# Performance work log

Hardware: AMD Instinct MI355X
Metric: run time of the kernel (lower is better)

Reference implementation:

```python
import jax, jax.numpy as jnp
import numpy as np

COMMITMENT_COST = 0.25


def setup_inputs() -> dict:
    key = jax.random.key(0)
    k1, k2 = jax.random.split(key)
    z = jax.random.normal(k1, (16, 64, 64, 64), dtype=jnp.float32)  # [B, C=embed_dim, H, W]
    embedding = jax.random.normal(k2, (1024, 64), dtype=jnp.float32)  # [K, D]
    return {"z": z, "embedding": embedding}


def reference(z, embedding):
    B, C, H, W = z.shape
    K, D = embedding.shape
    # NCHW -> NHWC, flatten to [N, D]
    z_perm = jnp.transpose(z, (0, 2, 3, 1))
    z_flat = z_perm.reshape(-1, D)
    N = z_flat.shape[0]
    # squared L2 distances: ||z||^2 + ||e||^2 - 2 z e^T  -> [N, K]
    distances = (
        jnp.sum(z_flat ** 2, axis=1, keepdims=True)
        + jnp.sum(embedding ** 2, axis=1)
        - 2.0 * jnp.matmul(z_flat, embedding.T)
    )
    encoding_indices = jnp.argmin(distances, axis=1)  # [N]
    # gather instead of one-hot matmul (same math, efficient)
    quantized = embedding[encoding_indices].reshape(z_perm.shape)
    # commitment loss (eval-mode forward; EMA buffer updates are train-only side effects)
    e_latent_loss = jnp.mean((jax.lax.stop_gradient(quantized) - z_perm) ** 2)
    loss = COMMITMENT_COST * e_latent_loss
    # straight-through estimator
    quantized_st = z_perm + jax.lax.stop_gradient(quantized - z_perm)
    quantized_out = jnp.transpose(quantized_st, (0, 3, 1, 2))
    # perplexity from code usage histogram (== mean of one-hot encodings)
    avg_probs = jnp.zeros((K,), dtype=jnp.float32).at[encoding_indices].add(1.0) / N
    perplexity = jnp.exp(-jnp.sum(avg_probs * jnp.log(avg_probs + 1e-10)))
    return quantized_out, loss, encoding_indices.reshape(B, H, W), perplexity
```

## Files before the change

### kernel.cpp

```cpp
#include <hip/hip_runtime.h>
#include <math.h>


#define QOUT_SZ  4194304
#define LOSS_OFF QOUT_SZ
#define IDX_OFF  (QOUT_SZ + 1)
#define PERP_OFF (QOUT_SZ + 1 + 65536)

typedef _Float16 f16x8 __attribute__((ext_vector_type(8)));
typedef _Float16 f16x4 __attribute__((ext_vector_type(4)));
typedef float    f32x4 __attribute__((ext_vector_type(4)));

#define WS_EHI   0
#define WS_ELO   131072
#define WS_ESQ   262144
#define WS_HIST  266240
#define WS_LOSS  270336

__device__ __forceinline__ void gll16(const void* g, void* l) {
    __builtin_amdgcn_global_load_lds(
        (const __attribute__((address_space(1))) void*)g,
        (__attribute__((address_space(3))) void*)l, 16, 0, 0);
}

__global__ void vq_pre(const float* __restrict__ emb,
                       _Float16* __restrict__ ehi, _Float16* __restrict__ elo,
                       float* __restrict__ esq, float* __restrict__ hist) {
    const int t = threadIdx.x;
    const int g = blockIdx.x * 256 + t;
    float4 v = ((const float4*)emb)[g];
    float xs[4] = {v.x, v.y, v.z, v.w};
    f16x4 hi, lo;
    float ss = 0.f;
#pragma unroll
    for (int j = 0; j < 4; ++j) {
        _Float16 h = (_Float16)xs[j];
        hi[j] = h;
        lo[j] = (_Float16)((xs[j] - (float)h) * 4096.0f);
        ss = fmaf(xs[j], xs[j], ss);
    }
    ((f16x4*)ehi)[g] = hi;
    ((f16x4*)elo)[g] = lo;
    ss += __shfl_xor(ss, 1, 64);
    ss += __shfl_xor(ss, 2, 64);
    ss += __shfl_xor(ss, 4, 64);
    ss += __shfl_xor(ss, 8, 64);
    if ((t & 15) == 0) esq[g >> 4] = -0.5f * ss;
    if (blockIdx.x < 4) hist[blockIdx.x * 256 + t] = 0.f;
}

__launch_bounds__(256, 4)
__global__ void vq_main(const float* __restrict__ z,
                        const float* __restrict__ emb,
                        const _Float16* __restrict__ gehi,
                        const _Float16* __restrict__ gelo,
                        const float* __restrict__ gesq,
                        float* __restrict__ hist,
                        float* __restrict__ lossp,
                        float* __restrict__ out) {
    __shared__ __align__(16) char es[32768];
    __shared__ float esql[1024];
    __shared__ float candv[128];
    __shared__ int   candi[128];
    __shared__ int   idxs[64];
    __shared__ float redw[4];

    const int tid  = threadIdx.x;
    const int blk  = blockIdx.x;
    const int b    = blk >> 6;
    const int h    = blk & 63;
    const int lane = tid & 63;
    const int wv   = tid >> 6;
    const int pg   = wv & 1;
    const int ksel = wv >> 1;
    const int col  = lane & 15;
    const int g    = lane >> 4;

#pragma unroll
    for (int i = 0; i < 4; ++i) esql[tid + 256 * i] = gesq[tid + 256 * i];

    const float* zb = z + (size_t)b * 262144 + (size_t)h * 64;
    const float* zrow = zb + pg * 32 + col;
    f16x8 Ah[2][2], Al[2][2];
#pragma unroll
    for (int pt = 0; pt < 2; ++pt) {
#pragma unroll
        for (int m = 0; m < 2; ++m) {
#pragma unroll
            for (int j = 0; j < 8; ++j) {
                int c = m * 32 + g * 8 + j;
                float x = zrow[pt * 16 + (size_t)c * 4096];
                _Float16 hh = (_Float16)x;
                Ah[pt][m][j] = hh;
                Al[pt][m][j] = (_Float16)((x - (float)hh) * 4096.0f);
            }
        }
    }

    const char* gh = (const char*)gehi;
    const char* gl = (const char*)gelo;
    const int u0 = tid, u1 = tid + 256;
    const int c0 = u0 >> 3, c1 = u1 >> 3;
    const size_t so0 = (size_t)c0 * 128 + (size_t)(((u0 & 7) ^ (c0 & 7)) * 16);
    const size_t so1 = (size_t)c1 * 128 + (size_t)(((u1 & 7) ^ (c1 & 7)) * 16);
    char* const dA = es + wv * 1024;

#define STAGE(n, bb) do { \
        const size_t gb_ = (size_t)(n) * 8192; \
        char* d_ = dA + (bb) * 16384; \
        gll16(gh + gb_ + so0, d_);            \
        gll16(gh + gb_ + so1, d_ + 4096);     \
        gll16(gl + gb_ + so0, d_ + 8192);     \
        gll16(gl + gb_ + so1, d_ + 12288);    \
    } while (0)

    int rb[2][2];
#pragma unroll
    for (int ct = 0; ct < 2; ++ct) {
        int cl = ksel * 32 + ct * 16 + col;
#pragma unroll
        for (int m = 0; m < 2; ++m)
            rb[ct][m] = cl * 128 + ((((m * 4 + g) * 16)) ^ ((col & 7) << 4));
    }

    float best[2][4];
    int   besti[2][4];
#pragma unroll
    for (int pt = 0; pt < 2; ++pt)
#pragma unroll
        for (int r = 0; r < 4; ++r) { best[pt][r] = -3.4e38f; besti[pt][r] = 0; }

    STAGE(0, 0);

    for (int sc = 0; sc < 16; ++sc) {
        const int cur = sc & 1;
        asm volatile("s_waitcnt vmcnt(0)" ::: "memory");
        __builtin_amdgcn_s_barrier();
        asm volatile("" ::: "memory");
        if (sc < 15) STAGE(sc + 1, cur ^ 1);

        const char* bp = es + cur * 16384;
        const int kb = sc * 64 + ksel * 32;
#pragma unroll
        for (int ct = 0; ct < 2; ++ct) {
            const float e2  = esql[kb + ct * 16 + col];
            const int  kidx = kb + ct * 16 + col;
            f16x8 Bh0 = *(const f16x8*)(bp + rb[ct][0]);
            f16x8 Bh1 = *(const f16x8*)(bp + rb[ct][1]);
            f16x8 Bl0 = *(const f16x8*)(bp + 8192 + rb[ct][0]);
            f16x8 Bl1 = *(const f16x8*)(bp + 8192 + rb[ct][1]);
#pragma unroll
            for (int pt = 0; pt < 2; ++pt) {
                f32x4 ah = {e2, e2, e2, e2};
                f32x4 ax = {0.f, 0.f, 0.f, 0.f};
                ah = __builtin_amdgcn_mfma_f32_16x16x32_f16(Ah[pt][0], Bh0, ah, 0, 0, 0);
                ah = __builtin_amdgcn_mfma_f32_16x16x32_f16(Ah[pt][1], Bh1, ah, 0, 0, 0);
                ax = __builtin_amdgcn_mfma_f32_16x16x32_f16(Ah[pt][0], Bl0, ax, 0, 0, 0);
                ax = __builtin_amdgcn_mfma_f32_16x16x32_f16(Ah[pt][1], Bl1, ax, 0, 0, 0);
                ax = __builtin_amdgcn_mfma_f32_16x16x32_f16(Al[pt][0], Bh0, ax, 0, 0, 0);
                ax = __builtin_amdgcn_mfma_f32_16x16x32_f16(Al[pt][1], Bh1, ax, 0, 0, 0);
#pragma unroll
                for (int r = 0; r < 4; ++r) {
                    float mval = fmaf(0x1p-12f, ax[r], ah[r]);
                    if (mval > best[pt][r]) { best[pt][r] = mval; besti[pt][r] = kidx; }
                }
            }
        }
    }
#undef STAGE

#pragma unroll
    for (int mask = 1; mask <= 8; mask <<= 1) {
#pragma unroll
        for (int pt = 0; pt < 2; ++pt)
#pragma unroll
            for (int r = 0; r < 4; ++r) {
                float ov = __shfl_xor(best[pt][r], mask, 64);
                int   oi = __shfl_xor(besti[pt][r], mask, 64);
                if (ov > best[pt][r] ||
                    (ov == best[pt][r] && oi < besti[pt][r])) {
                    best[pt][r] = ov; besti[pt][r] = oi;
                }
            }
    }
    if (col == 0) {
#pragma unroll
        for (int pt = 0; pt < 2; ++pt)
#pragma unroll
            for (int r = 0; r < 4; ++r) {
                int p = pg * 32 + pt * 16 + g * 4 + r;
                candv[p * 2 + ksel] = best[pt][r];
                candi[p * 2 + ksel] = besti[pt][r];
            }
    }
    __syncthreads();

    if (tid < 64) {
        float v0 = candv[tid * 2],     v1 = candv[tid * 2 + 1];
        int   i0 = candi[tid * 2],     i1 = candi[tid * 2 + 1];
        int bi = (v1 > v0 || (v1 == v0 && i1 < i0)) ? i1 : i0;
        idxs[tid] = bi;
        atomicAdd(&hist[bi], 1.0f);
        out[(size_t)IDX_OFF + blk * 64 + tid] = (float)bi;
    }
    __syncthreads();

    const int w  = tid & 63;
    const int cq = tid >> 6;
    const int idx = idxs[w];
    const float* ev = emb + (size_t)idx * 64 + cq * 16;
    const float* zr = zb + w;
    float* outq = out + (size_t)b * 262144 + (size_t)h * 64 + w;
    float lsum = 0.f;
#pragma unroll
    for (int i = 0; i < 4; ++i) {
        float4 qv = *(const float4*)(ev + i * 4);
        float q4[4] = {qv.x, qv.y, qv.z, qv.w};
#pragma unroll
        for (int jj = 0; jj < 4; ++jj) {
            int c = cq * 16 + i * 4 + jj;
            float zv = zr[(size_t)c * 4096];
            outq[(size_t)c * 4096] = q4[jj];
            float d = q4[jj] - zv;
            lsum = fmaf(d, d, lsum);
        }
    }
#pragma unroll
    for (int off = 32; off > 0; off >>= 1)
        lsum += __shfl_xor(lsum, off, 64);
    if (lane == 0) redw[wv] = lsum;
    __syncthreads();
    if (tid == 0)
        lossp[blk] = redw[0] + redw[1] + redw[2] + redw[3];
}

__global__ void vq_fin(const float* __restrict__ hist,
                       const float* __restrict__ lossp,
                       float* __restrict__ out) {
    __shared__ float sh[1024];
    __shared__ float sl[1024];
    int t = threadIdx.x;
    float hc = hist[t];
    float p  = hc * (1.0f / 65536.0f);
    sh[t] = p * logf(p + 1e-10f);
    sl[t] = lossp[t];
    __syncthreads();
    for (int s = 512; s > 0; s >>= 1) {
        if (t < s) { sh[t] += sh[t + s]; sl[t] += sl[t + s]; }
        __syncthreads();
    }
    if (t == 0) {
        out[LOSS_OFF] = 0.25f * sl[0] / (float)QOUT_SZ;
        out[PERP_OFF] = expf(-sh[0]);
    }
}

extern "C" void kernel_launch(void* const* d_in, const int* in_sizes, int n_in,
                              void* d_out, int out_size, void* d_ws, size_t ws_size,
                              hipStream_t stream) {
    const float* z   = (const float*)d_in[0];
    const float* emb = (const float*)d_in[1];
    float* out = (float*)d_out;
    char*  ws  = (char*)d_ws;

    _Float16* ehi   = (_Float16*)(ws + WS_EHI);
    _Float16* elo   = (_Float16*)(ws + WS_ELO);
    float*    esq   = (float*)(ws + WS_ESQ);
    float*    hist  = (float*)(ws + WS_HIST);
    float*    lossp = (float*)(ws + WS_LOSS);

    vq_pre<<<64, 256, 0, stream>>>(emb, ehi, elo, esq, hist);
    vq_main<<<1024, 256, 0, stream>>>(z, emb, ehi, elo, esq, hist, lossp, out);
    vq_fin<<<1, 1024, 0, stream>>>(hist, lossp, out);
}
```

Measured before the change: 67.55 us.

## Enlarge VQ block to 256 points with triple-buffered codebook staging

```diff
diff --git a/kernel.cpp b/kernel.cpp
--- a/kernel.cpp
+++ b/kernel.cpp
@@ -49,7 +49,7 @@
     if (blockIdx.x < 4) hist[blockIdx.x * 256 + t] = 0.f;
 }
 
-__launch_bounds__(256, 4)
+__launch_bounds__(512, 2)
 __global__ void vq_main(const float* __restrict__ z,
                         const float* __restrict__ emb,
                         const _Float16* __restrict__ gehi,
@@ -58,38 +58,39 @@
                         float* __restrict__ hist,
                         float* __restrict__ lossp,
                         float* __restrict__ out) {
-    __shared__ __align__(16) char es[32768];
+    __shared__ __align__(16) char es[49152];
     __shared__ float esql[1024];
-    __shared__ float candv[128];
-    __shared__ int   candi[128];
-    __shared__ int   idxs[64];
-    __shared__ float redw[4];
+
+    float* candv = (float*)es;
+    int*   candi = (int*)(es + 2048);
+    int*   idxs  = (int*)(es + 4096);
+    float* redw  = (float*)(es + 5120);
 
     const int tid  = threadIdx.x;
     const int blk  = blockIdx.x;
-    const int b    = blk >> 6;
-    const int h    = blk & 63;
+    const int b    = blk >> 4;
+    const int h0   = (blk & 15) << 2;
     const int lane = tid & 63;
     const int wv   = tid >> 6;
-    const int pg   = wv & 1;
-    const int ksel = wv >> 1;
+    const int q    = wv >> 1;
+    const int ksel = wv & 1;
     const int col  = lane & 15;
     const int g    = lane >> 4;
 
-#pragma unroll
-    for (int i = 0; i < 4; ++i) esql[tid + 256 * i] = gesq[tid + 256 * i];
-
-    const float* zb = z + (size_t)b * 262144 + (size_t)h * 64;
-    const float* zrow = zb + pg * 32 + col;
-    f16x8 Ah[2][2], Al[2][2];
-#pragma unroll
-    for (int pt = 0; pt < 2; ++pt) {
+    esql[tid]       = gesq[tid];
+    esql[tid + 512] = gesq[tid + 512];
+
+    const float* zb = z + (size_t)b * 262144 + (size_t)h0 * 64;
+    const float* zrw = zb + q * 64 + col;
+    f16x8 Ah[4][2], Al[4][2];
+#pragma unroll
+    for (int pt = 0; pt < 4; ++pt) {
 #pragma unroll
         for (int m = 0; m < 2; ++m) {
 #pragma unroll
             for (int j = 0; j < 8; ++j) {
                 int c = m * 32 + g * 8 + j;
-                float x = zrow[pt * 16 + (size_t)c * 4096];
+                float x = zrw[pt * 16 + (size_t)c * 4096];
                 _Float16 hh = (_Float16)x;
                 Ah[pt][m][j] = hh;
                 Al[pt][m][j] = (_Float16)((x - (float)hh) * 4096.0f);
@@ -99,19 +100,14 @@
 
     const char* gh = (const char*)gehi;
     const char* gl = (const char*)gelo;
-    const int u0 = tid, u1 = tid + 256;
-    const int c0 = u0 >> 3, c1 = u1 >> 3;
-    const size_t so0 = (size_t)c0 * 128 + (size_t)(((u0 & 7) ^ (c0 & 7)) * 16);
-    const size_t so1 = (size_t)c1 * 128 + (size_t)(((u1 & 7) ^ (c1 & 7)) * 16);
-    char* const dA = es + wv * 1024;
-
-#define STAGE(n, bb) do { \
+    const int   cc = tid >> 3;
+    const size_t so = (size_t)cc * 128 + (size_t)(((tid & 7) ^ (cc & 7)) << 4);
+    const int dofs = wv * 1024;
+
+#define STAGE(n, bo) do { \
         const size_t gb_ = (size_t)(n) * 8192; \
-        char* d_ = dA + (bb) * 16384; \
-        gll16(gh + gb_ + so0, d_);            \
-        gll16(gh + gb_ + so1, d_ + 4096);     \
-        gll16(gl + gb_ + so0, d_ + 8192);     \
-        gll16(gl + gb_ + so1, d_ + 12288);    \
+        gll16(gh + gb_ + so, es + (bo) + dofs);          \
+        gll16(gl + gb_ + so, es + (bo) + 8192 + dofs);   \
     } while (0)
 
     int rb[2][2];
@@ -120,37 +116,43 @@
         int cl = ksel * 32 + ct * 16 + col;
 #pragma unroll
         for (int m = 0; m < 2; ++m)
-            rb[ct][m] = cl * 128 + ((((m * 4 + g) * 16)) ^ ((col & 7) << 4));
-    }
-
-    float best[2][4];
-    int   besti[2][4];
-#pragma unroll
-    for (int pt = 0; pt < 2; ++pt)
+            rb[ct][m] = cl * 128 + ((((m << 2) + g) ^ (cl & 7)) << 4);
+    }
+
+    float best[4][4];
+    int   besti[4][4];
+#pragma unroll
+    for (int pt = 0; pt < 4; ++pt)
 #pragma unroll
         for (int r = 0; r < 4; ++r) { best[pt][r] = -3.4e38f; besti[pt][r] = 0; }
 
+    __syncthreads();
     STAGE(0, 0);
-
+    STAGE(1, 16384);
+
+    int cur = 0;
     for (int sc = 0; sc < 16; ++sc) {
-        const int cur = sc & 1;
-        asm volatile("s_waitcnt vmcnt(0)" ::: "memory");
+        if (sc < 15) asm volatile("s_waitcnt vmcnt(2)" ::: "memory");
+        else         asm volatile("s_waitcnt vmcnt(0)" ::: "memory");
         __builtin_amdgcn_s_barrier();
         asm volatile("" ::: "memory");
-        if (sc < 15) STAGE(sc + 1, cur ^ 1);
-
-        const char* bp = es + cur * 16384;
+        if (sc < 14) {
+            int st = cur + 32768; if (st >= 49152) st -= 49152;
+            STAGE(sc + 2, st);
+        }
+
+        const char* bp = es + cur;
         const int kb = sc * 64 + ksel * 32;
 #pragma unroll
         for (int ct = 0; ct < 2; ++ct) {
-            const float e2  = esql[kb + ct * 16 + col];
-            const int  kidx = kb + ct * 16 + col;
+            const int  kcol = kb + ct * 16 + col;
+            const float e2  = esql[kcol];
             f16x8 Bh0 = *(const f16x8*)(bp + rb[ct][0]);
             f16x8 Bh1 = *(const f16x8*)(bp + rb[ct][1]);
             f16x8 Bl0 = *(const f16x8*)(bp + 8192 + rb[ct][0]);
             f16x8 Bl1 = *(const f16x8*)(bp + 8192 + rb[ct][1]);
 #pragma unroll
-            for (int pt = 0; pt < 2; ++pt) {
+            for (int pt = 0; pt < 4; ++pt) {
                 f32x4 ah = {e2, e2, e2, e2};
                 f32x4 ax = {0.f, 0.f, 0.f, 0.f};
                 ah = __builtin_amdgcn_mfma_f32_16x16x32_f16(Ah[pt][0], Bh0, ah, 0, 0, 0);
@@ -162,17 +164,18 @@
 #pragma unroll
                 for (int r = 0; r < 4; ++r) {
                     float mval = fmaf(0x1p-12f, ax[r], ah[r]);
-                    if (mval > best[pt][r]) { best[pt][r] = mval; besti[pt][r] = kidx; }
+                    if (mval > best[pt][r]) { best[pt][r] = mval; besti[pt][r] = kcol; }
                 }
             }
         }
+        cur += 16384; if (cur >= 49152) cur = 0;
     }
 #undef STAGE
 
 #pragma unroll
     for (int mask = 1; mask <= 8; mask <<= 1) {
 #pragma unroll
-        for (int pt = 0; pt < 2; ++pt)
+        for (int pt = 0; pt < 4; ++pt)
 #pragma unroll
             for (int r = 0; r < 4; ++r) {
                 float ov = __shfl_xor(best[pt][r], mask, 64);
@@ -183,42 +186,45 @@
                 }
             }
     }
+    __syncthreads();
     if (col == 0) {
 #pragma unroll
-        for (int pt = 0; pt < 2; ++pt)
+        for (int pt = 0; pt < 4; ++pt)
 #pragma unroll
             for (int r = 0; r < 4; ++r) {
-                int p = pg * 32 + pt * 16 + g * 4 + r;
+                int p = q * 64 + pt * 16 + g * 4 + r;
                 candv[p * 2 + ksel] = best[pt][r];
                 candi[p * 2 + ksel] = besti[pt][r];
             }
     }
     __syncthreads();
 
-    if (tid < 64) {
+    if (tid < 256) {
         float v0 = candv[tid * 2],     v1 = candv[tid * 2 + 1];
         int   i0 = candi[tid * 2],     i1 = candi[tid * 2 + 1];
         int bi = (v1 > v0 || (v1 == v0 && i1 < i0)) ? i1 : i0;
         idxs[tid] = bi;
         atomicAdd(&hist[bi], 1.0f);
-        out[(size_t)IDX_OFF + blk * 64 + tid] = (float)bi;
+        out[(size_t)IDX_OFF + (size_t)blk * 256 + tid] = (float)bi;
     }
     __syncthreads();
 
     const int w  = tid & 63;
-    const int cq = tid >> 6;
-    const int idx = idxs[w];
-    const float* ev = emb + (size_t)idx * 64 + cq * 16;
-    const float* zr = zb + w;
-    float* outq = out + (size_t)b * 262144 + (size_t)h * 64 + w;
+    const int hh = (tid >> 6) & 3;
+    const int cq = tid >> 8;
+    const int pl = hh * 64 + w;
+    const int idx = idxs[pl];
+    const float* ev = emb + (size_t)idx * 64 + cq * 32;
+    const float* zr = zb + hh * 64 + w;
+    float* outq = out + (size_t)b * 262144 + (size_t)(h0 + hh) * 64 + w;
     float lsum = 0.f;
 #pragma unroll
-    for (int i = 0; i < 4; ++i) {
+    for (int i = 0; i < 8; ++i) {
         float4 qv = *(const float4*)(ev + i * 4);
         float q4[4] = {qv.x, qv.y, qv.z, qv.w};
 #pragma unroll
         for (int jj = 0; jj < 4; ++jj) {
-            int c = cq * 16 + i * 4 + jj;
+            int c = cq * 32 + i * 4 + jj;
             float zv = zr[(size_t)c * 4096];
             outq[(size_t)c * 4096] = q4[jj];
             float d = q4[jj] - zv;
@@ -230,8 +236,12 @@
         lsum += __shfl_xor(lsum, off, 64);
     if (lane == 0) redw[wv] = lsum;
     __syncthreads();
-    if (tid == 0)
-        lossp[blk] = redw[0] + redw[1] + redw[2] + redw[3];
+    if (tid == 0) {
+        float s = 0.f;
+#pragma unroll
+        for (int i = 0; i < 8; ++i) s += redw[i];
+        lossp[blk] = s;
+    }
 }
 
 __global__ void vq_fin(const float* __restrict__ hist,
@@ -243,7 +253,7 @@
     float hc = hist[t];
     float p  = hc * (1.0f / 65536.0f);
     sh[t] = p * logf(p + 1e-10f);
-    sl[t] = lossp[t];
+    sl[t] = (t < 256) ? lossp[t] : 0.f;
     __syncthreads();
     for (int s = 512; s > 0; s >>= 1) {
         if (t < s) { sh[t] += sh[t + s]; sl[t] += sl[t + s]; }
@@ -270,6 +280,6 @@
     float*    lossp = (float*)(ws + WS_LOSS);
 
     vq_pre<<<64, 256, 0, stream>>>(emb, ehi, elo, esq, hist);
-    vq_main<<<1024, 256, 0, stream>>>(z, emb, ehi, elo, esq, hist, lossp, out);
+    vq_main<<<256, 512, 0, stream>>>(z, emb, ehi, elo, esq, hist, lossp, out);
     vq_fin<<<1, 1024, 0, stream>>>(hist, lossp, out);
 }
```

Measured after the change: 75.40 us. 1.12x slower.

## Stream codebook directly into registers and give each wave the full codebook

Applied to the files above, without the earlier changes.

```diff
diff --git a/kernel.cpp b/kernel.cpp
--- a/kernel.cpp
+++ b/kernel.cpp
@@ -16,12 +16,6 @@
 #define WS_ESQ   262144
 #define WS_HIST  266240
 #define WS_LOSS  270336
-
-__device__ __forceinline__ void gll16(const void* g, void* l) {
-    __builtin_amdgcn_global_load_lds(
-        (const __attribute__((address_space(1))) void*)g,
-        (__attribute__((address_space(3))) void*)l, 16, 0, 0);
-}
 
 __global__ void vq_pre(const float* __restrict__ emb,
                        _Float16* __restrict__ ehi, _Float16* __restrict__ elo,
@@ -49,7 +43,7 @@
     if (blockIdx.x < 4) hist[blockIdx.x * 256 + t] = 0.f;
 }
 
-__launch_bounds__(256, 4)
+__launch_bounds__(256, 2)
 __global__ void vq_main(const float* __restrict__ z,
                         const float* __restrict__ emb,
                         const _Float16* __restrict__ gehi,
@@ -58,29 +52,22 @@
                         float* __restrict__ hist,
                         float* __restrict__ lossp,
                         float* __restrict__ out) {
-    __shared__ __align__(16) char es[32768];
-    __shared__ float esql[1024];
-    __shared__ float candv[128];
-    __shared__ int   candi[128];
-    __shared__ int   idxs[64];
+    __shared__ int   idxs[128];
     __shared__ float redw[4];
 
     const int tid  = threadIdx.x;
     const int blk  = blockIdx.x;
-    const int b    = blk >> 6;
-    const int h    = blk & 63;
+    const int b    = blk >> 5;
+    const int h0   = (blk & 31) << 1;
     const int lane = tid & 63;
     const int wv   = tid >> 6;
-    const int pg   = wv & 1;
-    const int ksel = wv >> 1;
+    const int hf   = wv >> 1;
+    const int wside= (wv & 1) << 5;
     const int col  = lane & 15;
     const int g    = lane >> 4;
 
-#pragma unroll
-    for (int i = 0; i < 4; ++i) esql[tid + 256 * i] = gesq[tid + 256 * i];
-
-    const float* zb = z + (size_t)b * 262144 + (size_t)h * 64;
-    const float* zrow = zb + pg * 32 + col;
+    const float* zb = z + (size_t)b * 262144 + (size_t)h0 * 64;
+    const float* zrw = zb + hf * 64 + wside + col;
     f16x8 Ah[2][2], Al[2][2];
 #pragma unroll
     for (int pt = 0; pt < 2; ++pt) {
@@ -89,7 +76,7 @@
 #pragma unroll
             for (int j = 0; j < 8; ++j) {
                 int c = m * 32 + g * 8 + j;
-                float x = zrow[pt * 16 + (size_t)c * 4096];
+                float x = zrw[pt * 16 + (size_t)c * 4096];
                 _Float16 hh = (_Float16)x;
                 Ah[pt][m][j] = hh;
                 Al[pt][m][j] = (_Float16)((x - (float)hh) * 4096.0f);
@@ -97,31 +84,52 @@
         }
     }
 
+    const int inv = col * 128 + g * 16;
     const char* gh = (const char*)gehi;
     const char* gl = (const char*)gelo;
-    const int u0 = tid, u1 = tid + 256;
-    const int c0 = u0 >> 3, c1 = u1 >> 3;
-    const size_t so0 = (size_t)c0 * 128 + (size_t)(((u0 & 7) ^ (c0 & 7)) * 16);
-    const size_t so1 = (size_t)c1 * 128 + (size_t)(((u1 & 7) ^ (c1 & 7)) * 16);
-    char* const dA = es + wv * 1024;
-
-#define STAGE(n, bb) do { \
-        const size_t gb_ = (size_t)(n) * 8192; \
-        char* d_ = dA + (bb) * 16384; \
-        gll16(gh + gb_ + so0, d_);            \
-        gll16(gh + gb_ + so1, d_ + 4096);     \
-        gll16(gl + gb_ + so0, d_ + 8192);     \
-        gll16(gl + gb_ + so1, d_ + 12288);    \
+
+    f16x8 B0h[2][2], B0l[2][2], B1h[2][2], B1l[2][2];
+    float Q0[2], Q1[2];
+
+#define LOADB(BH, BL, QQ, n) do {                                         \
+        const int nb_ = (n) * 4096;                                       \
+        _Pragma("unroll")                                                  \
+        for (int ct_ = 0; ct_ < 2; ++ct_) {                                \
+            _Pragma("unroll")                                              \
+            for (int m_ = 0; m_ < 2; ++m_) {                               \
+                const int o_ = nb_ + ct_ * 2048 + m_ * 64 + inv;           \
+                BH[ct_][m_] = *(const f16x8*)(gh + o_);                    \
+                BL[ct_][m_] = *(const f16x8*)(gl + o_);                    \
+            }                                                              \
+            QQ[ct_] = gesq[(n) * 32 + ct_ * 16 + col];                     \
+        }                                                                  \
     } while (0)
 
-    int rb[2][2];
-#pragma unroll
-    for (int ct = 0; ct < 2; ++ct) {
-        int cl = ksel * 32 + ct * 16 + col;
-#pragma unroll
-        for (int m = 0; m < 2; ++m)
-            rb[ct][m] = cl * 128 + ((((m * 4 + g) * 16)) ^ ((col & 7) << 4));
-    }
+#define COMPUTE(BH, BL, QQ, n) do {                                       \
+        _Pragma("unroll")                                                  \
+        for (int ct_ = 0; ct_ < 2; ++ct_) {                                \
+            const float e2_  = QQ[ct_];                                    \
+            const int   kidx_ = (n) * 32 + ct_ * 16 + col;                 \
+            _Pragma("unroll")                                              \
+            for (int pt_ = 0; pt_ < 2; ++pt_) {                            \
+                f32x4 ah_ = {e2_, e2_, e2_, e2_};                          \
+                f32x4 ax_ = {0.f, 0.f, 0.f, 0.f};                          \
+                ah_ = __builtin_amdgcn_mfma_f32_16x16x32_f16(Ah[pt_][0], BH[ct_][0], ah_, 0, 0, 0); \
+                ah_ = __builtin_amdgcn_mfma_f32_16x16x32_f16(Ah[pt_][1], BH[ct_][1], ah_, 0, 0, 0); \
+                ax_ = __builtin_amdgcn_mfma_f32_16x16x32_f16(Ah[pt_][0], BL[ct_][0], ax_, 0, 0, 0); \
+                ax_ = __builtin_amdgcn_mfma_f32_16x16x32_f16(Ah[pt_][1], BL[ct_][1], ax_, 0, 0, 0); \
+                ax_ = __builtin_amdgcn_mfma_f32_16x16x32_f16(Al[pt_][0], BH[ct_][0], ax_, 0, 0, 0); \
+                ax_ = __builtin_amdgcn_mfma_f32_16x16x32_f16(Al[pt_][1], BH[ct_][1], ax_, 0, 0, 0); \
+                _Pragma("unroll")                                          \
+                for (int r_ = 0; r_ < 4; ++r_) {                           \
+                    float mv_ = fmaf(0x1p-12f, ax_[r_], ah_[r_]);          \
+                    if (mv_ > best[pt_][r_]) {                             \
+                        best[pt_][r_] = mv_; besti[pt_][r_] = kidx_;       \
+                    }                                                      \
+                }                                                          \
+            }                                                              \
+        }                                                                  \
+    } while (0)
 
     float best[2][4];
     int   besti[2][4];
@@ -130,44 +138,18 @@
 #pragma unroll
         for (int r = 0; r < 4; ++r) { best[pt][r] = -3.4e38f; besti[pt][r] = 0; }
 
-    STAGE(0, 0);
-
-    for (int sc = 0; sc < 16; ++sc) {
-        const int cur = sc & 1;
-        asm volatile("s_waitcnt vmcnt(0)" ::: "memory");
-        __builtin_amdgcn_s_barrier();
-        asm volatile("" ::: "memory");
-        if (sc < 15) STAGE(sc + 1, cur ^ 1);
-
-        const char* bp = es + cur * 16384;
-        const int kb = sc * 64 + ksel * 32;
-#pragma unroll
-        for (int ct = 0; ct < 2; ++ct) {
-            const float e2  = esql[kb + ct * 16 + col];
-            const int  kidx = kb + ct * 16 + col;
-            f16x8 Bh0 = *(const f16x8*)(bp + rb[ct][0]);
-            f16x8 Bh1 = *(const f16x8*)(bp + rb[ct][1]);
-            f16x8 Bl0 = *(const f16x8*)(bp + 8192 + rb[ct][0]);
-            f16x8 Bl1 = *(const f16x8*)(bp + 8192 + rb[ct][1]);
-#pragma unroll
-            for (int pt = 0; pt < 2; ++pt) {
-                f32x4 ah = {e2, e2, e2, e2};
-                f32x4 ax = {0.f, 0.f, 0.f, 0.f};
-                ah = __builtin_amdgcn_mfma_f32_16x16x32_f16(Ah[pt][0], Bh0, ah, 0, 0, 0);
-                ah = __builtin_amdgcn_mfma_f32_16x16x32_f16(Ah[pt][1], Bh1, ah, 0, 0, 0);
-                ax = __builtin_amdgcn_mfma_f32_16x16x32_f16(Ah[pt][0], Bl0, ax, 0, 0, 0);
-                ax = __builtin_amdgcn_mfma_f32_16x16x32_f16(Ah[pt][1], Bl1, ax, 0, 0, 0);
-                ax = __builtin_amdgcn_mfma_f32_16x16x32_f16(Al[pt][0], Bh0, ax, 0, 0, 0);
-                ax = __builtin_amdgcn_mfma_f32_16x16x32_f16(Al[pt][1], Bh1, ax, 0, 0, 0);
-#pragma unroll
-                for (int r = 0; r < 4; ++r) {
-                    float mval = fmaf(0x1p-12f, ax[r], ah[r]);
-                    if (mval > best[pt][r]) { best[pt][r] = mval; besti[pt][r] = kidx; }
-                }
-            }
-        }
-    }
-#undef STAGE
+    LOADB(B0h, B0l, Q0, 0);
+    for (int sc = 0; sc < 30; sc += 2) {
+        LOADB(B1h, B1l, Q1, sc + 1);
+        COMPUTE(B0h, B0l, Q0, sc);
+        LOADB(B0h, B0l, Q0, sc + 2);
+        COMPUTE(B1h, B1l, Q1, sc + 1);
+    }
+    LOADB(B1h, B1l, Q1, 31);
+    COMPUTE(B0h, B0l, Q0, 30);
+    COMPUTE(B1h, B1l, Q1, 31);
+#undef LOADB
+#undef COMPUTE
 
 #pragma unroll
     for (int mask = 1; mask <= 8; mask <<= 1) {
@@ -187,42 +169,38 @@
 #pragma unroll
         for (int pt = 0; pt < 2; ++pt)
 #pragma unroll
-            for (int r = 0; r < 4; ++r) {
-                int p = pg * 32 + pt * 16 + g * 4 + r;
-                candv[p * 2 + ksel] = best[pt][r];
-                candi[p * 2 + ksel] = besti[pt][r];
-            }
+            for (int r = 0; r < 4; ++r)
+                idxs[hf * 64 + wside + pt * 16 + g * 4 + r] = besti[pt][r];
     }
     __syncthreads();
 
-    if (tid < 64) {
-        float v0 = candv[tid * 2],     v1 = candv[tid * 2 + 1];
-        int   i0 = candi[tid * 2],     i1 = candi[tid * 2 + 1];
-        int bi = (v1 > v0 || (v1 == v0 && i1 < i0)) ? i1 : i0;
-        idxs[tid] = bi;
+    if (tid < 128) {
+        int bi = idxs[tid];
         atomicAdd(&hist[bi], 1.0f);
-        out[(size_t)IDX_OFF + blk * 64 + tid] = (float)bi;
-    }
-    __syncthreads();
+        out[(size_t)IDX_OFF + (size_t)blk * 128 + tid] = (float)bi;
+    }
 
     const int w  = tid & 63;
     const int cq = tid >> 6;
-    const int idx = idxs[w];
-    const float* ev = emb + (size_t)idx * 64 + cq * 16;
-    const float* zr = zb + w;
-    float* outq = out + (size_t)b * 262144 + (size_t)h * 64 + w;
     float lsum = 0.f;
 #pragma unroll
-    for (int i = 0; i < 4; ++i) {
-        float4 qv = *(const float4*)(ev + i * 4);
-        float q4[4] = {qv.x, qv.y, qv.z, qv.w};
-#pragma unroll
-        for (int jj = 0; jj < 4; ++jj) {
-            int c = cq * 16 + i * 4 + jj;
-            float zv = zr[(size_t)c * 4096];
-            outq[(size_t)c * 4096] = q4[jj];
-            float d = q4[jj] - zv;
-            lsum = fmaf(d, d, lsum);
+    for (int h2 = 0; h2 < 2; ++h2) {
+        const int idx = idxs[h2 * 64 + w];
+        const float* ev = emb + (size_t)idx * 64 + cq * 16;
+        const float* zr = zb + h2 * 64 + w;
+        float* outq = out + (size_t)b * 262144 + (size_t)(h0 + h2) * 64 + w;
+#pragma unroll
+        for (int i = 0; i < 4; ++i) {
+            float4 qv = *(const float4*)(ev + i * 4);
+            float q4[4] = {qv.x, qv.y, qv.z, qv.w};
+#pragma unroll
+            for (int jj = 0; jj < 4; ++jj) {
+                int c = cq * 16 + i * 4 + jj;
+                float zv = zr[(size_t)c * 4096];
+                outq[(size_t)c * 4096] = q4[jj];
+                float d = q4[jj] - zv;
+                lsum = fmaf(d, d, lsum);
+            }
         }
     }
 #pragma unroll
@@ -243,7 +221,7 @@
     float hc = hist[t];
     float p  = hc * (1.0f / 65536.0f);
     sh[t] = p * logf(p + 1e-10f);
-    sl[t] = lossp[t];
+    sl[t] = (t < 512) ? lossp[t] : 0.f;
     __syncthreads();
     for (int s = 512; s > 0; s >>= 1) {
         if (t < s) { sh[t] += sh[t + s]; sl[t] += sl[t + s]; }
@@ -270,6 +248,6 @@
     float*    lossp = (float*)(ws + WS_LOSS);
 
     vq_pre<<<64, 256, 0, stream>>>(emb, ehi, elo, esq, hist);
-    vq_main<<<1024, 256, 0, stream>>>(z, emb, ehi, elo, esq, hist, lossp, out);
+    vq_main<<<512, 256, 0, stream>>>(z, emb, ehi, elo, esq, hist, lossp, out);
     vq_fin<<<1, 1024, 0, stream>>>(hist, lossp, out);
 }
```

Measured after the change: 102.3 us. 51.5% more time.

## Triple-buffer codebook staging with two-ahead prefetch and alias scratch into LDS

Applied to the files above, without the earlier changes.

```diff
diff --git a/kernel.cpp b/kernel.cpp
--- a/kernel.cpp
+++ b/kernel.cpp
@@ -49,7 +49,7 @@
     if (blockIdx.x < 4) hist[blockIdx.x * 256 + t] = 0.f;
 }
 
-__launch_bounds__(256, 4)
+__launch_bounds__(256, 3)
 __global__ void vq_main(const float* __restrict__ z,
                         const float* __restrict__ emb,
                         const _Float16* __restrict__ gehi,
@@ -58,12 +58,13 @@
                         float* __restrict__ hist,
                         float* __restrict__ lossp,
                         float* __restrict__ out) {
-    __shared__ __align__(16) char es[32768];
+    __shared__ __align__(16) char es[49152];
     __shared__ float esql[1024];
-    __shared__ float candv[128];
-    __shared__ int   candi[128];
-    __shared__ int   idxs[64];
-    __shared__ float redw[4];
+
+    float* candv = (float*)(es + 16384);
+    int*   candi = (int*)(es + 16384 + 512);
+    int*   idxs  = (int*)(es + 16384 + 1024);
+    float* redw  = (float*)(es + 16384 + 1280);
 
     const int tid  = threadIdx.x;
     const int blk  = blockIdx.x;
@@ -105,9 +106,9 @@
     const size_t so1 = (size_t)c1 * 128 + (size_t)(((u1 & 7) ^ (c1 & 7)) * 16);
     char* const dA = es + wv * 1024;
 
-#define STAGE(n, bb) do { \
+#define STAGE(n, bo) do { \
         const size_t gb_ = (size_t)(n) * 8192; \
-        char* d_ = dA + (bb) * 16384; \
+        char* d_ = dA + (bo); \
         gll16(gh + gb_ + so0, d_);            \
         gll16(gh + gb_ + so1, d_ + 4096);     \
         gll16(gl + gb_ + so0, d_ + 8192);     \
@@ -120,7 +121,7 @@
         int cl = ksel * 32 + ct * 16 + col;
 #pragma unroll
         for (int m = 0; m < 2; ++m)
-            rb[ct][m] = cl * 128 + ((((m * 4 + g) * 16)) ^ ((col & 7) << 4));
+            rb[ct][m] = cl * 128 + ((((m << 2) + g) ^ (cl & 7)) << 4);
     }
 
     float best[2][4];
@@ -130,21 +131,33 @@
 #pragma unroll
         for (int r = 0; r < 4; ++r) { best[pt][r] = -3.4e38f; besti[pt][r] = 0; }
 
+    __syncthreads();
     STAGE(0, 0);
+    STAGE(1, 16384);
 
     for (int sc = 0; sc < 16; ++sc) {
-        const int cur = sc & 1;
-        asm volatile("s_waitcnt vmcnt(0)" ::: "memory");
+        if (sc < 15) asm volatile("s_waitcnt vmcnt(4)" ::: "memory");
+        else         asm volatile("s_waitcnt vmcnt(0)" ::: "memory");
         __builtin_amdgcn_s_barrier();
         asm volatile("" ::: "memory");
-        if (sc < 15) STAGE(sc + 1, cur ^ 1);
-
-        const char* bp = es + cur * 16384;
+        if (sc < 14) {
+            int st = sc + 2; st -= (st >= 3) ? 3 : 0; st -= (st >= 3) ? 3 : 0;
+        }
+        {
+            int nxt = sc + 2;
+            if (nxt < 16) {
+                int bo = nxt - (nxt / 3) * 3;
+                STAGE(nxt, bo * 16384);
+            }
+        }
+
+        const int cb = sc - (sc / 3) * 3;
+        const char* bp = es + cb * 16384;
         const int kb = sc * 64 + ksel * 32;
 #pragma unroll
         for (int ct = 0; ct < 2; ++ct) {
-            const float e2  = esql[kb + ct * 16 + col];
-            const int  kidx = kb + ct * 16 + col;
+            const int  kcol = kb + ct * 16 + col;
+            const float e2  = esql[kcol];
             f16x8 Bh0 = *(const f16x8*)(bp + rb[ct][0]);
             f16x8 Bh1 = *(const f16x8*)(bp + rb[ct][1]);
             f16x8 Bl0 = *(const f16x8*)(bp + 8192 + rb[ct][0]);
@@ -162,7 +175,7 @@
 #pragma unroll
                 for (int r = 0; r < 4; ++r) {
                     float mval = fmaf(0x1p-12f, ax[r], ah[r]);
-                    if (mval > best[pt][r]) { best[pt][r] = mval; besti[pt][r] = kidx; }
+                    if (mval > best[pt][r]) { best[pt][r] = mval; besti[pt][r] = kcol; }
                 }
             }
         }
```

New measurement: 73.79 us. 9.2% more time.
